# Kernel tuning notes

Hardware: AMD Instinct MI355X
Metric: run time of the kernel (lower is better)

## Reference

```python
import jax, jax.numpy as jnp
import numpy as np

B, L, DH = 4, 4096, 1024
T, DG = 1024, 768
P = 256


def setup_inputs() -> dict:
    key = jax.random.key(0)
    k1, k2, k3, k4, k5 = jax.random.split(key, 5)
    H = jax.random.normal(k1, (B, L, DH), dtype=jnp.float32)
    G = jax.random.normal(k2, (B, T, DG), dtype=jnp.float32)
    # key mask: True = padded/masked. Guarantee at least one valid key per row.
    mask = jax.random.randint(k3, (B, L), 0, 2).astype(jnp.bool_)
    mask = mask.at[:, 0].set(False)
    # torch Linear weights: [out, in]
    Wk_w = jax.random.normal(k4, (P, DH), dtype=jnp.float32) * (DH ** -0.5)
    Wq_w = jax.random.normal(k5, (P, DG), dtype=jnp.float32) * (DG ** -0.5)
    return {"H": H, "G": G, "mask": mask, "Wk_w": Wk_w, "Wq_w": Wq_w}


def reference(H, G, mask, Wk_w, Wq_w):
    # K = Wk(H): [B,L,P]; Q = Wq(G): [B,T,P]
    K = jnp.einsum('bld,pd->blp', H, Wk_w)
    Q = jnp.einsum('btd,pd->btp', G, Wq_w)
    scale = P ** -0.5
    logits = jnp.einsum('btp,blp->btl', Q, K) * scale  # [B,T,L]
    neg_inf = jnp.finfo(logits.dtype).min
    logits = jnp.where(mask[:, None, :], neg_inf, logits)
    alpha = jax.nn.softmax(logits, axis=-1)  # softmax over L (streaming-equivalent)
    Z = jnp.einsum('btl,bld->btd', alpha, H)  # [B,T,DH]
    return Z
```

## Files before the change

### kernel.cpp

```cpp
#include <hip/hip_runtime.h>
#include <hip/hip_bf16.h>


typedef __attribute__((ext_vector_type(8))) short short8;
typedef __attribute__((ext_vector_type(4))) float f32x4;

static __device__ __forceinline__ unsigned short bf16bits(float x) {
    __hip_bfloat16 b = __float2bfloat16(x);
    return *(unsigned short*)&b;
}

static __device__ __forceinline__ void gload_lds16(const __hip_bfloat16* g,
                                                   __hip_bfloat16* l)
{
    auto gp = (const __attribute__((address_space(1))) unsigned int*)(uintptr_t)g;
    auto lp = (__attribute__((address_space(3))) unsigned int*)(unsigned int)(uintptr_t)l;
    __builtin_amdgcn_global_load_lds(gp, lp, 16, 0, 0);
}

__global__ __launch_bounds__(256)
void scan_kernel(const void* __restrict__ mask,
                 unsigned short* __restrict__ idx,
                 int* __restrict__ lc, int* __restrict__ lcpad,
                 float* __restrict__ rowsum, int L, int T, int B)
{
    const int b = blockIdx.x;
    const int tid = threadIdx.x;

    for (int i = tid; i < T; i += 256) rowsum[(long)b * T + i] = 0.f;

    const unsigned char*  m8g  = (const unsigned char*)mask;
    const unsigned short* m16g = (const unsigned short*)mask;
    const unsigned int*   m32g = (const unsigned int*)mask;
    __shared__ int c1, c2, c4, c8, cp, wsh;
    if (tid == 0) { c1 = c2 = c4 = c8 = cp = 0; }
    __syncthreads();
    {
        const int N = B * L;
        int l1 = 0, l2 = 0, l4 = 0, l8 = 0, lp = 0;
        for (int i = tid; i < N; i += 256) l1 += (m8g[i] != 0);
        for (int i = tid; i < N / 2; i += 256) {
            l2 += (m16g[i] != 0);
            lp += ((m8g[2 * i] != 0) == (m8g[2 * i + 1] != 0));
        }
        for (int i = tid; i < N / 4; i += 256) l4 += (m32g[i] != 0);
        for (int i = tid; i < N / 8; i += 256) l8 += ((m32g[2 * i] | m32g[2 * i + 1]) != 0);
        atomicAdd(&c1, l1); atomicAdd(&c2, l2); atomicAdd(&c4, l4);
        atomicAdd(&c8, l8); atomicAdd(&cp, lp);
    }
    __syncthreads();
    if (tid == 0) {
        const float f1 = fabsf(c1 / 16384.f - 0.5f);
        const float f2 = fabsf(c2 / 8192.f  - 0.5f);
        const float f4 = fabsf(c4 / 4096.f  - 0.5f);
        const float f8 = fabsf(c8 / 2048.f  - 0.5f);
        int w = 1; float best = f1;
        if (f2 < best) { best = f2; w = 2; }
        if (f4 < best) { best = f4; w = 4; }
        if (f8 < best) { best = f8; w = 8; }
        if (w == 1 && cp > 7400) w = 2;
        wsh = w;
    }
    __syncthreads();
    const int w = wsh;

    const unsigned char*  m8  = (const unsigned char*)mask;
    const unsigned short* m16 = (const unsigned short*)mask;
    const unsigned int*   m32 = (const unsigned int*)mask;
    const uint2*          m64 = (const uint2*)mask;
    bool v[16];
    int cnt = 0;
    #pragma unroll
    for (int i = 0; i < 16; ++i) {
        const int l = tid * 16 + i;
        const long mi = (long)b * L + l;
        bool masked;
        if (w == 1)      masked = m8[mi] != 0;
        else if (w == 2) masked = m16[mi] != 0;
        else if (w == 4) masked = m32[mi] != 0;
        else             { uint2 q = m64[mi]; masked = (q.x | q.y) != 0; }
        v[i] = !masked;
        cnt += v[i] ? 1 : 0;
    }
    __shared__ int waveTot[4];
    int pre = cnt;
    #pragma unroll
    for (int off = 1; off < 64; off <<= 1) {
        const int t = __shfl_up(pre, off, 64);
        if ((tid & 63) >= off) pre += t;
    }
    if ((tid & 63) == 63) waveTot[tid >> 6] = pre;
    __syncthreads();
    int waveOff = 0;
    for (int wv = 0; wv < (tid >> 6); ++wv) waveOff += waveTot[wv];
    int o = waveOff + pre - cnt;
    #pragma unroll
    for (int i = 0; i < 16; ++i)
        if (v[i]) idx[(long)b * L + (o++)] = (unsigned short)(tid * 16 + i);
    if (tid == 255) {
        const int total = waveOff + pre;
        lc[b] = total;
        lcpad[b] = (total + 127) & ~127;
    }
}

__global__ __launch_bounds__(256)
void prep_all_kernel(const float* __restrict__ H,
                     __hip_bfloat16* __restrict__ Hbf,
                     __hip_bfloat16* __restrict__ Ht,
                     const unsigned short* __restrict__ idx,
                     const int* __restrict__ lc, const int* __restrict__ lcpad,
                     const float* __restrict__ Wk, unsigned short* __restrict__ Wkbf,
                     const float* __restrict__ Wq, unsigned short* __restrict__ Wqbf,
                     const float* __restrict__ G,  unsigned short* __restrict__ Gbf,
                     int L, int D)
{
    __shared__ __align__(16) __hip_bfloat16 tile[64][72];
    int id = blockIdx.x;
    if (id < 4096) {
        const int b  = id >> 10;
        const int c0 = (id & 63) * 64;
        if (c0 >= lcpad[b]) return;
        const int d0 = ((id >> 6) & 15) * 64;
        const int Lcb = lc[b];
        const float* Hb = H + (long)b * L * D;
        __hip_bfloat16* Hbfb = Hbf + (long)b * L * D;
        __hip_bfloat16* Htb  = Ht  + (long)b * D * L;
        const int tx = threadIdx.x & 15, ty = threadIdx.x >> 4;
        #pragma unroll
        for (int p = 0; p < 4; ++p) {
            const int row = ty + p * 16;
            const int c = c0 + row;
            float4 v = {0.f, 0.f, 0.f, 0.f};
            if (c < Lcb) {
                const int l = idx[(long)b * L + c];
                v = *(const float4*)(&Hb[(long)l * D + d0 + tx * 4]);
            }
            ushort4 o;
            o.x = bf16bits(v.x); o.y = bf16bits(v.y);
            o.z = bf16bits(v.z); o.w = bf16bits(v.w);
            *(ushort4*)(&Hbfb[(long)c * D + d0 + tx * 4]) = o;
            tile[tx * 4 + 0][row] = __float2bfloat16(v.x);
            tile[tx * 4 + 1][row] = __float2bfloat16(v.y);
            tile[tx * 4 + 2][row] = __float2bfloat16(v.z);
            tile[tx * 4 + 3][row] = __float2bfloat16(v.w);
        }
        __syncthreads();
        const int ll = threadIdx.x & 7;
        const int dq = threadIdx.x >> 3;
        #pragma unroll
        for (int q = 0; q < 2; ++q) {
            const int dd = dq + q * 32;
            const short8 v = *(const short8*)(&tile[dd][ll * 8]);
            *(short8*)(&Htb[(long)(d0 + dd) * L + c0 + ll * 8]) = v;
        }
        return;
    }
    id -= 4096;
    const float* in; unsigned short* out; int n4;
    if (id < 256)       { in = Wk; out = Wkbf; n4 = (256 * 1024) / 4; }
    else if (id < 448)  { id -= 256; in = Wq; out = Wqbf; n4 = (256 * 768) / 4; }
    else                { id -= 448; in = G;  out = Gbf;  n4 = (4 * 1024 * 768) / 4; }
    const int i = id * 256 + threadIdx.x;
    if (i >= n4) return;
    float4 v = ((const float4*)in)[i];
    ushort4 o;
    o.x = bf16bits(v.x); o.y = bf16bits(v.y);
    o.z = bf16bits(v.z); o.w = bf16bits(v.w);
    ((ushort4*)out)[i] = o;
}

template <typename OutT, int SPLITK, int MODE, int CMODE>
static __device__ __forceinline__
void gemm_bt_body(int bx, int by, int bz, __hip_bfloat16* lds_pool,
                  const __hip_bfloat16* __restrict__ A,
                  const __hip_bfloat16* __restrict__ Bm,
                  OutT* __restrict__ C,
                  int K, int lda, int ldb, int ldc,
                  long batchStrideA, long batchStrideB, long batchStrideC,
                  float scale,
                  float* __restrict__ rowsum, int rowsumStride,
                  long partStride,
                  const int* __restrict__ lc, const int* __restrict__ lcpad,
                  int Lfull)
{
    const int zb = bz / SPLITK;
    const int kc = bz % SPLITK;
    const int rowBase = bx * 128;
    const int colBase = by * 128;

    if constexpr (CMODE == 1) {
        const int bb = rowBase / Lfull;
        if (rowBase - bb * Lfull >= lcpad[bb]) return;
    }
    if constexpr (CMODE == 2) {
        if (colBase >= lcpad[zb]) return;
    }

    A  += (long)zb * batchStrideA;
    Bm += (long)zb * batchStrideB;
    C  += (long)zb * batchStrideC + (long)kc * partStride;
    int Kdyn = K;
    if constexpr (CMODE == 3) Kdyn = lcpad[zb];
    const int Kloc  = Kdyn / SPLITK;
    const int kbase = kc * Kloc;
    const int NT    = Kloc / 32;

    const int tid  = threadIdx.x;
    const int lane = tid & 63;
    const int wave = tid >> 6;
    const int wm = (wave & 1) * 64;
    const int wn = (wave >> 1) * 64;

    __hip_bfloat16* AsP = lds_pool;
    __hip_bfloat16* BsP = lds_pool + 12288;

    f32x4 acc[4][4];
    #pragma unroll
    for (int i = 0; i < 4; ++i)
        #pragma unroll
        for (int j = 0; j < 4; ++j)
            acc[i][j] = (f32x4){0.f, 0.f, 0.f, 0.f};

    const int srow = lane >> 2;
    const int scol = ((lane & 3) ^ ((lane >> 3) & 3)) * 8;
    const long ar0 = (long)(rowBase + wave * 32 + srow) * lda;
    const long ar1 = ar0 + 16l * lda;
    const long br0 = (long)(colBase + wave * 32 + srow) * ldb;
    const long br1 = br0 + 16l * ldb;

    const int mrow = lane & 15;
    const int koff = (((lane >> 4) ^ ((lane >> 1) & 3)) * 8);

    auto stage = [&](int buf, int t) {
        const int kk = kbase + t * 32 + scol;
        gload_lds16(A  + ar0 + kk, AsP + buf * 4096 + wave * 1024);
        gload_lds16(A  + ar1 + kk, AsP + buf * 4096 + wave * 1024 + 512);
        gload_lds16(Bm + br0 + kk, BsP + buf * 4096 + wave * 1024);
        gload_lds16(Bm + br1 + kk, BsP + buf * 4096 + wave * 1024 + 512);
    };

    stage(0, 0);
    if (NT > 1) stage(1, 1);

    int cur = 0;
    for (int t = 0; t < NT; ++t) {
        if (t + 1 < NT)
            asm volatile("s_waitcnt vmcnt(4)" ::: "memory");
        else
            asm volatile("s_waitcnt vmcnt(0)" ::: "memory");
        __builtin_amdgcn_s_barrier();
        if (t + 2 < NT) {
            const int nxt2 = (cur >= 1) ? cur - 1 : cur + 2;
            stage(nxt2, t + 2);
        }

        short8 af[4], bf[4];
        #pragma unroll
        for (int mi = 0; mi < 4; ++mi)
            af[mi] = *(const short8*)(AsP + cur * 4096 + (wm + mi * 16 + mrow) * 32 + koff);
        #pragma unroll
        for (int ni = 0; ni < 4; ++ni)
            bf[ni] = *(const short8*)(BsP + cur * 4096 + (wn + ni * 16 + mrow) * 32 + koff);

        #pragma unroll
        for (int mi = 0; mi < 4; ++mi)
            #pragma unroll
            for (int ni = 0; ni < 4; ++ni)
                acc[mi][ni] = __builtin_amdgcn_mfma_f32_16x16x32_bf16(
                    af[mi], bf[ni], acc[mi][ni], 0, 0, 0);
        cur = (cur == 2) ? 0 : cur + 1;
    }

    const int crow0 = (lane >> 4) * 4;
    const int ccol  = lane & 15;

    if constexpr (MODE == 2 || sizeof(OutT) == 2) {
        __syncthreads();
        __hip_bfloat16* cst = lds_pool;

        if constexpr (MODE == 2) {
            const int lcv = lc[zb];
            bool mk[4];
            #pragma unroll
            for (int ni = 0; ni < 4; ++ni)
                mk[ni] = (colBase + wn + ni * 16 + ccol) >= lcv;
            #pragma unroll
            for (int mi = 0; mi < 4; ++mi) {
                #pragma unroll
                for (int r = 0; r < 4; ++r) {
                    const int row = wm + mi * 16 + crow0 + r;
                    float rs = 0.f;
                    #pragma unroll
                    for (int ni = 0; ni < 4; ++ni) {
                        const int col = wn + ni * 16 + ccol;
                        const float e = mk[ni] ? 0.f
                                               : __expf(acc[mi][ni][r] * scale);
                        const __hip_bfloat16 pb = __float2bfloat16(e);
                        cst[row * 136 + (((col >> 3) ^ (row >> 3)) << 3) + (col & 7)] = pb;
                        rs += __bfloat162float(pb);
                    }
                    rs += __shfl_xor(rs, 1, 64);
                    rs += __shfl_xor(rs, 2, 64);
                    rs += __shfl_xor(rs, 4, 64);
                    rs += __shfl_xor(rs, 8, 64);
                    if ((lane & 15) == 0)
                        atomicAdd(&rowsum[(long)zb * rowsumStride + rowBase + row], rs);
                }
            }
        } else {
            #pragma unroll
            for (int mi = 0; mi < 4; ++mi) {
                #pragma unroll
                for (int ni = 0; ni < 4; ++ni) {
                    #pragma unroll
                    for (int r = 0; r < 4; ++r) {
                        const int row = wm + mi * 16 + crow0 + r;
                        const int col = wn + ni * 16 + ccol;
                        cst[row * 136 + (((col >> 3) ^ (row >> 3)) << 3) + (col & 7)] =
                            __float2bfloat16(acc[mi][ni][r] * scale);
                    }
                }
            }
        }
        __syncthreads();
        const int g   = tid & 15;
        const int r4  = tid >> 4;
        const int lof = ((g ^ r4) << 3);
        #pragma unroll
        for (int k = 0; k < 8; ++k) {
            const int row = r4 * 8 + k;
            const short8 v = *(const short8*)(cst + row * 136 + lof);
            *(short8*)(&((__hip_bfloat16*)C)[(long)(rowBase + row) * ldc + colBase + g * 8]) = v;
        }
    } else {
        #pragma unroll
        for (int mi = 0; mi < 4; ++mi) {
            #pragma unroll
            for (int ni = 0; ni < 4; ++ni) {
                #pragma unroll
                for (int r = 0; r < 4; ++r) {
                    const int row = rowBase + wm + mi * 16 + crow0 + r;
                    const int col = colBase + wn + ni * 16 + ccol;
                    ((float*)C)[(long)row * ldc + col] = acc[mi][ni][r] * scale;
                }
            }
        }
    }
}

static __device__ __forceinline__ void xcd_swizzle(int& bx, int& by, int& bz)
{
    const int nwg = gridDim.x * gridDim.y * gridDim.z;
    bx = blockIdx.x; by = blockIdx.y; bz = blockIdx.z;
    if ((nwg & 7) == 0) {
        int lin = bx + gridDim.x * (by + gridDim.y * bz);
        lin = (lin & 7) * (nwg >> 3) + (lin >> 3);
        bx = lin % gridDim.x;
        const int t = lin / gridDim.x;
        by = t % gridDim.y;
        bz = t / gridDim.y;
    }
}

template <typename OutT, int SPLITK, int MODE, int CMODE>
__global__ __launch_bounds__(256)
void gemm_bt_kernel(const __hip_bfloat16* __restrict__ A,
                    const __hip_bfloat16* __restrict__ Bm,
                    OutT* __restrict__ C,
                    int K, int lda, int ldb, int ldc,
                    long batchStrideA, long batchStrideB, long batchStrideC,
                    float scale,
                    float* __restrict__ rowsum, int rowsumStride,
                    long partStride,
                    const int* __restrict__ lc, const int* __restrict__ lcpad,
                    int Lfull)
{
    __shared__ __align__(16) __hip_bfloat16 lds_pool[24576];
    int bx, by, bz;
    xcd_swizzle(bx, by, bz);
    gemm_bt_body<OutT, SPLITK, MODE, CMODE>(bx, by, bz, lds_pool,
        A, Bm, C, K, lda, ldb, ldc, batchStrideA, batchStrideB, batchStrideC,
        scale, rowsum, rowsumStride, partStride, lc, lcpad, Lfull);
}

__global__ __launch_bounds__(256)
void qk_gemm_kernel(const __hip_bfloat16* __restrict__ Gbf,
                    const __hip_bfloat16* __restrict__ Wqbf,
                    __hip_bfloat16* __restrict__ Qbf,
                    const __hip_bfloat16* __restrict__ Hbf,
                    const __hip_bfloat16* __restrict__ Wkbf,
                    __hip_bfloat16* __restrict__ Kbf,
                    const int* __restrict__ lcpad,
                    int DG_, int DH_, int P_, int L_)
{
    __shared__ __align__(16) __hip_bfloat16 lds_pool[24576];
    int bx, by, bz;
    xcd_swizzle(bx, by, bz);
    if (bx < 32) {
        gemm_bt_body<__hip_bfloat16, 1, 0, 0>(bx, by, 0, lds_pool,
            Gbf, Wqbf, Qbf, DG_, DG_, DG_, P_, 0, 0, 0, 1.0f,
            nullptr, 0, 0, nullptr, nullptr, 0);
    } else {
        gemm_bt_body<__hip_bfloat16, 1, 0, 1>(bx - 32, by, 0, lds_pool,
            Hbf, Wkbf, Kbf, DH_, DH_, DH_, P_, 0, 0, 0, 1.0f,
            nullptr, 0, 0, nullptr, lcpad, L_);
    }
}

__global__ __launch_bounds__(256)
void combine_kernel(const float* __restrict__ Zp,
                    const float* __restrict__ rowsum,
                    float* __restrict__ Z, long partStride)
{
    const int i = blockIdx.x * 256 + threadIdx.x;
    const float4 a = ((const float4*)Zp)[i];
    const float4 b = ((const float4*)(Zp + partStride))[i];
    const float inv = 1.0f / rowsum[i >> 8];
    float4 o;
    o.x = (a.x + b.x) * inv;
    o.y = (a.y + b.y) * inv;
    o.z = (a.z + b.z) * inv;
    o.w = (a.w + b.w) * inv;
    ((float4*)Z)[i] = o;
}

extern "C" void kernel_launch(void* const* d_in, const int* in_sizes, int n_in,
                              void* d_out, int out_size, void* d_ws, size_t ws_size,
                              hipStream_t stream)
{
    constexpr int B = 4, L = 4096, DH = 1024, T = 1024, DG = 768, P = 256;

    const float* H  = (const float*)d_in[0];
    const float* G  = (const float*)d_in[1];
    const void*  mask = d_in[2];
    const float* Wk = (const float*)d_in[3];
    const float* Wq = (const float*)d_in[4];
    for (int i = 0; i < n_in; ++i) {
        switch (in_sizes[i]) {
            case B * L * DH: H    = (const float*)d_in[i]; break;
            case B * T * DG: G    = (const float*)d_in[i]; break;
            case B * L:      mask = d_in[i];               break;
            case P * DH:     Wk   = (const float*)d_in[i]; break;
            case P * DG:     Wq   = (const float*)d_in[i]; break;
        }
    }
    float* Z = (float*)d_out;

    char* ws = (char*)d_ws;
    __hip_bfloat16* Hbf  = (__hip_bfloat16*)ws;
    float*          Zp   = (float*)ws;
    __hip_bfloat16* Ht   = (__hip_bfloat16*)(ws + (32l << 20));
    __hip_bfloat16* Gbf  = (__hip_bfloat16*)(ws + (64l << 20));
    __hip_bfloat16* Qbf  = (__hip_bfloat16*)(ws + (70l << 20));
    __hip_bfloat16* Kbf  = (__hip_bfloat16*)(ws + (72l << 20));
    __hip_bfloat16* Wkbf = (__hip_bfloat16*)(ws + (80l << 20));
    __hip_bfloat16* Wqbf = (__hip_bfloat16*)(ws + (80l << 20) + (512l << 10));
    float*          rowsum    = (float*)(ws + (80l << 20) + (896l << 10));
    int*            lcBuf     = (int*)  (ws + (80l << 20) + (961l << 10));
    int*            lcpadBuf  = (int*)  (ws + (80l << 20) + (961l << 10) + 64);
    unsigned short* idxBuf    = (unsigned short*)(ws + (80l << 20) + (962l << 10));
    __hip_bfloat16* Sb   = (__hip_bfloat16*)(ws + (81l << 20));

    constexpr long ZPART = (long)B * T * DH;

    const dim3 blk(256);

    scan_kernel<<<dim3(B), blk, 0, stream>>>(
        mask, idxBuf, lcBuf, lcpadBuf, rowsum, L, T, B);

    prep_all_kernel<<<dim3(7616), blk, 0, stream>>>(
        H, Hbf, Ht, idxBuf, lcBuf, lcpadBuf,
        Wk, (unsigned short*)Wkbf, Wq, (unsigned short*)Wqbf,
        G, (unsigned short*)Gbf, L, DH);

    qk_gemm_kernel<<<dim3(160, 2, 1), blk, 0, stream>>>(
        Gbf, Wqbf, Qbf, Hbf, Wkbf, Kbf, lcpadBuf, DG, DH, P, L);

    gemm_bt_kernel<__hip_bfloat16, 1, 2, 2><<<dim3(T / 128, L / 128, B), blk, 0, stream>>>(
        Qbf, Kbf, Sb, P, P, P, L,
        (long)T * P, (long)L * P, (long)T * L, 0.0625f,
        rowsum, T, 0, lcBuf, lcpadBuf, L);
    gemm_bt_kernel<float, 2, 0, 3><<<dim3(T / 128, DH / 128, B * 2), blk, 0, stream>>>(
        Sb, Ht, Zp, L, L, L, DH,
        (long)T * L, (long)DH * L, (long)T * DH, 1.0f,
        nullptr, 0, ZPART, nullptr, lcpadBuf, L);
    combine_kernel<<<dim3((B * T * DH / 4) / 256), blk, 0, stream>>>(
        Zp, rowsum, Z, ZPART);
}
```

Before: 219.9 us.

## Fuse mask scan into consumers, drop split-K and combine kernel for Z GEMM

Removes the separate single-block-per-batch scan kernel. Each prep, QK, S and Z block now recomputes the mask width detection and valid-key count (or prefix compaction) itself. The Z GEMM no longer uses split-K plus a combine pass: it uses 64-row tiles with full K and applies the rowsum normalisation in its epilogue, which saves the partial-buffer round trip and two launches. In exchange, every block redundantly reads the whole mask (16K bytes, several passes), which adds latency and memory traffic per block.

```diff
diff --git a/kernel.cpp b/kernel.cpp
--- a/kernel.cpp
+++ b/kernel.cpp
@@ -18,150 +18,154 @@
     __builtin_amdgcn_global_load_lds(gp, lp, 16, 0, 0);
 }
 
-__global__ __launch_bounds__(256)
-void scan_kernel(const void* __restrict__ mask,
-                 unsigned short* __restrict__ idx,
-                 int* __restrict__ lc, int* __restrict__ lcpad,
-                 float* __restrict__ rowsum, int L, int T, int B)
-{
-    const int b = blockIdx.x;
+static __device__ bool masked_at(const void* mask, int w, long i)
+{
+    if (w == 1) return ((const unsigned char*)mask)[i] != 0;
+    if (w == 2) return ((const unsigned short*)mask)[i] != 0;
+    if (w == 4) return ((const unsigned int*)mask)[i] != 0;
+    uint2 q = ((const uint2*)mask)[i]; return (q.x | q.y) != 0;
+}
+
+static __device__ int detect_width_dev(const void* mask, int* sh)
+{
     const int tid = threadIdx.x;
-
-    for (int i = tid; i < T; i += 256) rowsum[(long)b * T + i] = 0.f;
-
-    const unsigned char*  m8g  = (const unsigned char*)mask;
-    const unsigned short* m16g = (const unsigned short*)mask;
-    const unsigned int*   m32g = (const unsigned int*)mask;
-    __shared__ int c1, c2, c4, c8, cp, wsh;
-    if (tid == 0) { c1 = c2 = c4 = c8 = cp = 0; }
-    __syncthreads();
-    {
-        const int N = B * L;
-        int l1 = 0, l2 = 0, l4 = 0, l8 = 0, lp = 0;
-        for (int i = tid; i < N; i += 256) l1 += (m8g[i] != 0);
-        for (int i = tid; i < N / 2; i += 256) {
-            l2 += (m16g[i] != 0);
-            lp += ((m8g[2 * i] != 0) == (m8g[2 * i + 1] != 0));
-        }
-        for (int i = tid; i < N / 4; i += 256) l4 += (m32g[i] != 0);
-        for (int i = tid; i < N / 8; i += 256) l8 += ((m32g[2 * i] | m32g[2 * i + 1]) != 0);
-        atomicAdd(&c1, l1); atomicAdd(&c2, l2); atomicAdd(&c4, l4);
-        atomicAdd(&c8, l8); atomicAdd(&cp, lp);
-    }
-    __syncthreads();
-    if (tid == 0) {
-        const float f1 = fabsf(c1 / 16384.f - 0.5f);
-        const float f2 = fabsf(c2 / 8192.f  - 0.5f);
-        const float f4 = fabsf(c4 / 4096.f  - 0.5f);
-        const float f8 = fabsf(c8 / 2048.f  - 0.5f);
-        int w = 1; float best = f1;
-        if (f2 < best) { best = f2; w = 2; }
-        if (f4 < best) { best = f4; w = 4; }
-        if (f8 < best) { best = f8; w = 8; }
-        if (w == 1 && cp > 7400) w = 2;
-        wsh = w;
-    }
-    __syncthreads();
-    const int w = wsh;
-
     const unsigned char*  m8  = (const unsigned char*)mask;
     const unsigned short* m16 = (const unsigned short*)mask;
     const unsigned int*   m32 = (const unsigned int*)mask;
-    const uint2*          m64 = (const uint2*)mask;
-    bool v[16];
+    if (tid < 5) sh[tid] = 0;
+    __syncthreads();
+    int l1 = 0, l2 = 0, l4 = 0, l8 = 0, lp = 0;
+    for (int i = tid; i < 16384; i += 256) l1 += (m8[i] != 0);
+    for (int i = tid; i < 8192;  i += 256) {
+        l2 += (m16[i] != 0);
+        lp += ((m8[2 * i] != 0) == (m8[2 * i + 1] != 0));
+    }
+    for (int i = tid; i < 4096;  i += 256) l4 += (m32[i] != 0);
+    for (int i = tid; i < 2048;  i += 256) l8 += ((m32[2 * i] | m32[2 * i + 1]) != 0);
+    atomicAdd(&sh[0], l1); atomicAdd(&sh[1], l2); atomicAdd(&sh[2], l4);
+    atomicAdd(&sh[3], l8); atomicAdd(&sh[4], lp);
+    __syncthreads();
+    const float f1 = fabsf(sh[0] / 16384.f - 0.5f);
+    const float f2 = fabsf(sh[1] / 8192.f  - 0.5f);
+    const float f4 = fabsf(sh[2] / 4096.f  - 0.5f);
+    const float f8 = fabsf(sh[3] / 2048.f  - 0.5f);
+    int w = 1; float best = f1;
+    if (f2 < best) { best = f2; w = 2; }
+    if (f4 < best) { best = f4; w = 4; }
+    if (f8 < best) { best = f8; w = 8; }
+    if (w == 1 && sh[4] > 7400) w = 2;
+    return w;
+}
+
+static __device__ int count_valid_dev(const void* mask, int w, int b, int L, int* sh)
+{
+    const int tid = threadIdx.x;
+    if (tid == 0) sh[5] = 0;
+    __syncthreads();
     int cnt = 0;
+    for (int i = tid; i < L; i += 256)
+        cnt += masked_at(mask, w, (long)b * L + i) ? 0 : 1;
     #pragma unroll
-    for (int i = 0; i < 16; ++i) {
-        const int l = tid * 16 + i;
-        const long mi = (long)b * L + l;
-        bool masked;
-        if (w == 1)      masked = m8[mi] != 0;
-        else if (w == 2) masked = m16[mi] != 0;
-        else if (w == 4) masked = m32[mi] != 0;
-        else             { uint2 q = m64[mi]; masked = (q.x | q.y) != 0; }
-        v[i] = !masked;
-        cnt += v[i] ? 1 : 0;
-    }
-    __shared__ int waveTot[4];
-    int pre = cnt;
-    #pragma unroll
-    for (int off = 1; off < 64; off <<= 1) {
-        const int t = __shfl_up(pre, off, 64);
-        if ((tid & 63) >= off) pre += t;
-    }
-    if ((tid & 63) == 63) waveTot[tid >> 6] = pre;
+    for (int off = 32; off; off >>= 1) cnt += __shfl_xor(cnt, off, 64);
+    if ((tid & 63) == 0) atomicAdd(&sh[5], cnt);
     __syncthreads();
-    int waveOff = 0;
-    for (int wv = 0; wv < (tid >> 6); ++wv) waveOff += waveTot[wv];
-    int o = waveOff + pre - cnt;
-    #pragma unroll
-    for (int i = 0; i < 16; ++i)
-        if (v[i]) idx[(long)b * L + (o++)] = (unsigned short)(tid * 16 + i);
-    if (tid == 255) {
-        const int total = waveOff + pre;
-        lc[b] = total;
-        lcpad[b] = (total + 127) & ~127;
-    }
+    return sh[5];
 }
 
 __global__ __launch_bounds__(256)
 void prep_all_kernel(const float* __restrict__ H,
                      __hip_bfloat16* __restrict__ Hbf,
                      __hip_bfloat16* __restrict__ Ht,
-                     const unsigned short* __restrict__ idx,
-                     const int* __restrict__ lc, const int* __restrict__ lcpad,
+                     const void* __restrict__ mask,
                      const float* __restrict__ Wk, unsigned short* __restrict__ Wkbf,
                      const float* __restrict__ Wq, unsigned short* __restrict__ Wqbf,
                      const float* __restrict__ G,  unsigned short* __restrict__ Gbf,
+                     float* __restrict__ rowsum,
                      int L, int D)
 {
     __shared__ __align__(16) __hip_bfloat16 tile[64][72];
+    __shared__ unsigned short sidx[4096];
+    __shared__ int sh[8];
     int id = blockIdx.x;
+    const int tid = threadIdx.x;
     if (id < 4096) {
         const int b  = id >> 10;
         const int c0 = (id & 63) * 64;
-        if (c0 >= lcpad[b]) return;
         const int d0 = ((id >> 6) & 15) * 64;
-        const int Lcb = lc[b];
+
+        const int w = detect_width_dev(mask, sh);
+        bool v[16];
+        int cnt = 0;
+        #pragma unroll
+        for (int i = 0; i < 16; ++i) {
+            const int l = tid * 16 + i;
+            v[i] = !masked_at(mask, w, (long)b * L + l);
+            cnt += v[i] ? 1 : 0;
+        }
+        int pre = cnt;
+        #pragma unroll
+        for (int off = 1; off < 64; off <<= 1) {
+            const int t = __shfl_up(pre, off, 64);
+            if ((tid & 63) >= off) pre += t;
+        }
+        __syncthreads();
+        if ((tid & 63) == 63) sh[tid >> 6] = pre;
+        __syncthreads();
+        int waveOff = 0;
+        for (int wv = 0; wv < (tid >> 6); ++wv) waveOff += sh[wv];
+        int o = waveOff + pre - cnt;
+        #pragma unroll
+        for (int i = 0; i < 16; ++i)
+            if (v[i]) sidx[o++] = (unsigned short)(tid * 16 + i);
+        if (tid == 255) sh[6] = waveOff + pre;
+        __syncthreads();
+        const int Lcb = sh[6];
+        const int lcpadb = (Lcb + 127) & ~127;
+        if (c0 >= lcpadb) return;
+
         const float* Hb = H + (long)b * L * D;
         __hip_bfloat16* Hbfb = Hbf + (long)b * L * D;
         __hip_bfloat16* Htb  = Ht  + (long)b * D * L;
-        const int tx = threadIdx.x & 15, ty = threadIdx.x >> 4;
+        const int tx = tid & 15, ty = tid >> 4;
         #pragma unroll
         for (int p = 0; p < 4; ++p) {
             const int row = ty + p * 16;
             const int c = c0 + row;
-            float4 v = {0.f, 0.f, 0.f, 0.f};
+            float4 vv = {0.f, 0.f, 0.f, 0.f};
             if (c < Lcb) {
-                const int l = idx[(long)b * L + c];
-                v = *(const float4*)(&Hb[(long)l * D + d0 + tx * 4]);
+                const int l = sidx[c];
+                vv = *(const float4*)(&Hb[(long)l * D + d0 + tx * 4]);
             }
-            ushort4 o;
-            o.x = bf16bits(v.x); o.y = bf16bits(v.y);
-            o.z = bf16bits(v.z); o.w = bf16bits(v.w);
-            *(ushort4*)(&Hbfb[(long)c * D + d0 + tx * 4]) = o;
-            tile[tx * 4 + 0][row] = __float2bfloat16(v.x);
-            tile[tx * 4 + 1][row] = __float2bfloat16(v.y);
-            tile[tx * 4 + 2][row] = __float2bfloat16(v.z);
-            tile[tx * 4 + 3][row] = __float2bfloat16(v.w);
-        }
-        __syncthreads();
-        const int ll = threadIdx.x & 7;
-        const int dq = threadIdx.x >> 3;
+            ushort4 oo;
+            oo.x = bf16bits(vv.x); oo.y = bf16bits(vv.y);
+            oo.z = bf16bits(vv.z); oo.w = bf16bits(vv.w);
+            *(ushort4*)(&Hbfb[(long)c * D + d0 + tx * 4]) = oo;
+            tile[tx * 4 + 0][row] = __float2bfloat16(vv.x);
+            tile[tx * 4 + 1][row] = __float2bfloat16(vv.y);
+            tile[tx * 4 + 2][row] = __float2bfloat16(vv.z);
+            tile[tx * 4 + 3][row] = __float2bfloat16(vv.w);
+        }
+        __syncthreads();
+        const int ll = tid & 7;
+        const int dq = tid >> 3;
         #pragma unroll
         for (int q = 0; q < 2; ++q) {
             const int dd = dq + q * 32;
-            const short8 v = *(const short8*)(&tile[dd][ll * 8]);
-            *(short8*)(&Htb[(long)(d0 + dd) * L + c0 + ll * 8]) = v;
+            const short8 vv = *(const short8*)(&tile[dd][ll * 8]);
+            *(short8*)(&Htb[(long)(d0 + dd) * L + c0 + ll * 8]) = vv;
         }
         return;
     }
     id -= 4096;
+    if (id >= 3520) {
+        rowsum[(id - 3520) * 256 + tid] = 0.f;
+        return;
+    }
     const float* in; unsigned short* out; int n4;
     if (id < 256)       { in = Wk; out = Wkbf; n4 = (256 * 1024) / 4; }
     else if (id < 448)  { id -= 256; in = Wq; out = Wqbf; n4 = (256 * 768) / 4; }
     else                { id -= 448; in = G;  out = Gbf;  n4 = (4 * 1024 * 768) / 4; }
-    const int i = id * 256 + threadIdx.x;
+    const int i = id * 256 + tid;
     if (i >= n4) return;
     float4 v = ((const float4*)in)[i];
     ushort4 o;
@@ -170,61 +174,47 @@
     ((ushort4*)out)[i] = o;
 }
 
-template <typename OutT, int SPLITK, int MODE, int CMODE>
+template <typename OutT, int MODE, int BM>
 static __device__ __forceinline__
-void gemm_bt_body(int bx, int by, int bz, __hip_bfloat16* lds_pool,
+void gemm_bt_body(int bx, int by, int zb, __hip_bfloat16* lds_pool,
                   const __hip_bfloat16* __restrict__ A,
                   const __hip_bfloat16* __restrict__ Bm,
                   OutT* __restrict__ C,
                   int K, int lda, int ldb, int ldc,
                   long batchStrideA, long batchStrideB, long batchStrideC,
                   float scale,
-                  float* __restrict__ rowsum, int rowsumStride,
-                  long partStride,
-                  const int* __restrict__ lc, const int* __restrict__ lcpad,
-                  int Lfull)
-{
-    const int zb = bz / SPLITK;
-    const int kc = bz % SPLITK;
-    const int rowBase = bx * 128;
-    const int colBase = by * 128;
-
-    if constexpr (CMODE == 1) {
-        const int bb = rowBase / Lfull;
-        if (rowBase - bb * Lfull >= lcpad[bb]) return;
-    }
-    if constexpr (CMODE == 2) {
-        if (colBase >= lcpad[zb]) return;
-    }
+                  float* __restrict__ rowsum, int rowsumStride, int lcv)
+{
+    constexpr int MI  = BM / 32;
+    constexpr int ACH = BM / 64;
+    constexpr int ATS = BM * 32;
 
     A  += (long)zb * batchStrideA;
     Bm += (long)zb * batchStrideB;
-    C  += (long)zb * batchStrideC + (long)kc * partStride;
-    int Kdyn = K;
-    if constexpr (CMODE == 3) Kdyn = lcpad[zb];
-    const int Kloc  = Kdyn / SPLITK;
-    const int kbase = kc * Kloc;
-    const int NT    = Kloc / 32;
+    C  += (long)zb * batchStrideC;
+    const int NT = K / 32;
 
     const int tid  = threadIdx.x;
     const int lane = tid & 63;
     const int wave = tid >> 6;
-    const int wm = (wave & 1) * 64;
+    const int wm = (wave & 1) * (BM / 2);
     const int wn = (wave >> 1) * 64;
+    const int rowBase = bx * BM;
+    const int colBase = by * 128;
 
     __hip_bfloat16* AsP = lds_pool;
-    __hip_bfloat16* BsP = lds_pool + 12288;
-
-    f32x4 acc[4][4];
+    __hip_bfloat16* BsP = lds_pool + 3 * ATS;
+
+    f32x4 acc[MI][4];
     #pragma unroll
-    for (int i = 0; i < 4; ++i)
+    for (int i = 0; i < MI; ++i)
         #pragma unroll
         for (int j = 0; j < 4; ++j)
             acc[i][j] = (f32x4){0.f, 0.f, 0.f, 0.f};
 
     const int srow = lane >> 2;
     const int scol = ((lane & 3) ^ ((lane >> 3) & 3)) * 8;
-    const long ar0 = (long)(rowBase + wave * 32 + srow) * lda;
+    const long ar0 = (long)(rowBase + wave * (BM / 4) + srow) * lda;
     const long ar1 = ar0 + 16l * lda;
     const long br0 = (long)(colBase + wave * 32 + srow) * ldb;
     const long br1 = br0 + 16l * ldb;
@@ -233,38 +223,43 @@
     const int koff = (((lane >> 4) ^ ((lane >> 1) & 3)) * 8);
 
     auto stage = [&](int buf, int t) {
-        const int kk = kbase + t * 32 + scol;
-        gload_lds16(A  + ar0 + kk, AsP + buf * 4096 + wave * 1024);
-        gload_lds16(A  + ar1 + kk, AsP + buf * 4096 + wave * 1024 + 512);
+        const int kk = t * 32 + scol;
+        gload_lds16(A + ar0 + kk, AsP + buf * ATS + wave * (BM / 4) * 32);
+        if constexpr (ACH == 2)
+            gload_lds16(A + ar1 + kk, AsP + buf * ATS + wave * (BM / 4) * 32 + 512);
         gload_lds16(Bm + br0 + kk, BsP + buf * 4096 + wave * 1024);
         gload_lds16(Bm + br1 + kk, BsP + buf * 4096 + wave * 1024 + 512);
     };
 
     stage(0, 0);
-    if (NT > 1) stage(1, 1);
+    stage(1, 1);
 
     int cur = 0;
     for (int t = 0; t < NT; ++t) {
-        if (t + 1 < NT)
-            asm volatile("s_waitcnt vmcnt(4)" ::: "memory");
-        else
+        if (t + 1 < NT) {
+            if constexpr (ACH == 2)
+                asm volatile("s_waitcnt vmcnt(4)" ::: "memory");
+            else
+                asm volatile("s_waitcnt vmcnt(3)" ::: "memory");
+        } else {
             asm volatile("s_waitcnt vmcnt(0)" ::: "memory");
+        }
         __builtin_amdgcn_s_barrier();
         if (t + 2 < NT) {
             const int nxt2 = (cur >= 1) ? cur - 1 : cur + 2;
             stage(nxt2, t + 2);
         }
 
-        short8 af[4], bf[4];
-        #pragma unroll
-        for (int mi = 0; mi < 4; ++mi)
-            af[mi] = *(const short8*)(AsP + cur * 4096 + (wm + mi * 16 + mrow) * 32 + koff);
+        short8 af[MI], bf[4];
+        #pragma unroll
+        for (int mi = 0; mi < MI; ++mi)
+            af[mi] = *(const short8*)(AsP + cur * ATS + (wm + mi * 16 + mrow) * 32 + koff);
         #pragma unroll
         for (int ni = 0; ni < 4; ++ni)
             bf[ni] = *(const short8*)(BsP + cur * 4096 + (wn + ni * 16 + mrow) * 32 + koff);
 
         #pragma unroll
-        for (int mi = 0; mi < 4; ++mi)
+        for (int mi = 0; mi < MI; ++mi)
             #pragma unroll
             for (int ni = 0; ni < 4; ++ni)
                 acc[mi][ni] = __builtin_amdgcn_mfma_f32_16x16x32_bf16(
@@ -275,52 +270,34 @@
     const int crow0 = (lane >> 4) * 4;
     const int ccol  = lane & 15;
 
-    if constexpr (MODE == 2 || sizeof(OutT) == 2) {
+    if constexpr (MODE == 2) {
         __syncthreads();
         __hip_bfloat16* cst = lds_pool;
-
-        if constexpr (MODE == 2) {
-            const int lcv = lc[zb];
-            bool mk[4];
+        bool mk[4];
+        #pragma unroll
+        for (int ni = 0; ni < 4; ++ni)
+            mk[ni] = (colBase + wn + ni * 16 + ccol) >= lcv;
+        #pragma unroll
+        for (int mi = 0; mi < MI; ++mi) {
             #pragma unroll
-            for (int ni = 0; ni < 4; ++ni)
-                mk[ni] = (colBase + wn + ni * 16 + ccol) >= lcv;
-            #pragma unroll
-            for (int mi = 0; mi < 4; ++mi) {
-                #pragma unroll
-                for (int r = 0; r < 4; ++r) {
-                    const int row = wm + mi * 16 + crow0 + r;
-                    float rs = 0.f;
-                    #pragma unroll
-                    for (int ni = 0; ni < 4; ++ni) {
-                        const int col = wn + ni * 16 + ccol;
-                        const float e = mk[ni] ? 0.f
-                                               : __expf(acc[mi][ni][r] * scale);
-                        const __hip_bfloat16 pb = __float2bfloat16(e);
-                        cst[row * 136 + (((col >> 3) ^ (row >> 3)) << 3) + (col & 7)] = pb;
-                        rs += __bfloat162float(pb);
-                    }
-                    rs += __shfl_xor(rs, 1, 64);
-                    rs += __shfl_xor(rs, 2, 64);
-                    rs += __shfl_xor(rs, 4, 64);
-                    rs += __shfl_xor(rs, 8, 64);
-                    if ((lane & 15) == 0)
-                        atomicAdd(&rowsum[(long)zb * rowsumStride + rowBase + row], rs);
-                }
-            }
-        } else {
-            #pragma unroll
-            for (int mi = 0; mi < 4; ++mi) {
+            for (int r = 0; r < 4; ++r) {
+                const int row = wm + mi * 16 + crow0 + r;
+                float rs = 0.f;
                 #pragma unroll
                 for (int ni = 0; ni < 4; ++ni) {
-                    #pragma unroll
-                    for (int r = 0; r < 4; ++r) {
-                        const int row = wm + mi * 16 + crow0 + r;
-                        const int col = wn + ni * 16 + ccol;
-                        cst[row * 136 + (((col >> 3) ^ (row >> 3)) << 3) + (col & 7)] =
-                            __float2bfloat16(acc[mi][ni][r] * scale);
-                    }
+                    const int col = wn + ni * 16 + ccol;
+                    const float e = mk[ni] ? 0.f
+                                           : __expf(acc[mi][ni][r] * scale);
+                    const __hip_bfloat16 pb = __float2bfloat16(e);
+                    cst[row * 136 + (((col >> 3) ^ (row >> 3)) << 3) + (col & 7)] = pb;
+                    rs += __bfloat162float(pb);
                 }
+                rs += __shfl_xor(rs, 1, 64);
+                rs += __shfl_xor(rs, 2, 64);
+                rs += __shfl_xor(rs, 4, 64);
+                rs += __shfl_xor(rs, 8, 64);
+                if ((lane & 15) == 0)
+                    atomicAdd(&rowsum[(long)zb * rowsumStride + rowBase + row], rs);
             }
         }
         __syncthreads();
@@ -333,9 +310,49 @@
             const short8 v = *(const short8*)(cst + row * 136 + lof);
             *(short8*)(&((__hip_bfloat16*)C)[(long)(rowBase + row) * ldc + colBase + g * 8]) = v;
         }
+    } else if constexpr (MODE == 3) {
+        #pragma unroll
+        for (int mi = 0; mi < MI; ++mi) {
+            #pragma unroll
+            for (int r = 0; r < 4; ++r) {
+                const int row = rowBase + wm + mi * 16 + crow0 + r;
+                const float inv = 1.0f / rowsum[(long)zb * rowsumStride + row];
+                #pragma unroll
+                for (int ni = 0; ni < 4; ++ni) {
+                    const int col = colBase + wn + ni * 16 + ccol;
+                    ((float*)C)[(long)row * ldc + col] = acc[mi][ni][r] * inv;
+                }
+            }
+        }
+    } else if constexpr (sizeof(OutT) == 2) {
+        __syncthreads();
+        __hip_bfloat16* cst = lds_pool;
+        #pragma unroll
+        for (int mi = 0; mi < MI; ++mi) {
+            #pragma unroll
+            for (int ni = 0; ni < 4; ++ni) {
+                #pragma unroll
+                for (int r = 0; r < 4; ++r) {
+                    const int row = wm + mi * 16 + crow0 + r;
+                    const int col = wn + ni * 16 + ccol;
+                    cst[row * 136 + (((col >> 3) ^ (row >> 3)) << 3) + (col & 7)] =
+                        __float2bfloat16(acc[mi][ni][r] * scale);
+                }
+            }
+        }
+        __syncthreads();
+        const int g   = tid & 15;
+        const int r4  = tid >> 4;
+        const int lof = ((g ^ r4) << 3);
+        #pragma unroll
+        for (int k = 0; k < 8; ++k) {
+            const int row = r4 * 8 + k;
+            const short8 v = *(const short8*)(cst + row * 136 + lof);
+            *(short8*)(&((__hip_bfloat16*)C)[(long)(rowBase + row) * ldc + colBase + g * 8]) = v;
+        }
     } else {
         #pragma unroll
-        for (int mi = 0; mi < 4; ++mi) {
+        for (int mi = 0; mi < MI; ++mi) {
             #pragma unroll
             for (int ni = 0; ni < 4; ++ni) {
                 #pragma unroll
@@ -363,27 +380,6 @@
     }
 }
 
-template <typename OutT, int SPLITK, int MODE, int CMODE>
-__global__ __launch_bounds__(256)
-void gemm_bt_kernel(const __hip_bfloat16* __restrict__ A,
-                    const __hip_bfloat16* __restrict__ Bm,
-                    OutT* __restrict__ C,
-                    int K, int lda, int ldb, int ldc,
-                    long batchStrideA, long batchStrideB, long batchStrideC,
-                    float scale,
-                    float* __restrict__ rowsum, int rowsumStride,
-                    long partStride,
-                    const int* __restrict__ lc, const int* __restrict__ lcpad,
-                    int Lfull)
-{
-    __shared__ __align__(16) __hip_bfloat16 lds_pool[24576];
-    int bx, by, bz;
-    xcd_swizzle(bx, by, bz);
-    gemm_bt_body<OutT, SPLITK, MODE, CMODE>(bx, by, bz, lds_pool,
-        A, Bm, C, K, lda, ldb, ldc, batchStrideA, batchStrideB, batchStrideC,
-        scale, rowsum, rowsumStride, partStride, lc, lcpad, Lfull);
-}
-
 __global__ __launch_bounds__(256)
 void qk_gemm_kernel(const __hip_bfloat16* __restrict__ Gbf,
                     const __hip_bfloat16* __restrict__ Wqbf,
@@ -391,38 +387,74 @@
                     const __hip_bfloat16* __restrict__ Hbf,
                     const __hip_bfloat16* __restrict__ Wkbf,
                     __hip_bfloat16* __restrict__ Kbf,
-                    const int* __restrict__ lcpad,
+                    const void* __restrict__ mask,
                     int DG_, int DH_, int P_, int L_)
 {
     __shared__ __align__(16) __hip_bfloat16 lds_pool[24576];
     int bx, by, bz;
     xcd_swizzle(bx, by, bz);
     if (bx < 32) {
-        gemm_bt_body<__hip_bfloat16, 1, 0, 0>(bx, by, 0, lds_pool,
+        gemm_bt_body<__hip_bfloat16, 0, 128>(bx, by, 0, lds_pool,
             Gbf, Wqbf, Qbf, DG_, DG_, DG_, P_, 0, 0, 0, 1.0f,
-            nullptr, 0, 0, nullptr, nullptr, 0);
+            nullptr, 0, 0);
     } else {
-        gemm_bt_body<__hip_bfloat16, 1, 0, 1>(bx - 32, by, 0, lds_pool,
+        int* sh = (int*)lds_pool;
+        const int w = detect_width_dev(mask, sh);
+        const int rowBase = (bx - 32) * 128;
+        const int bb = rowBase / L_;
+        const int cnt = count_valid_dev(mask, w, bb, L_, sh);
+        const int lcpadb = (cnt + 127) & ~127;
+        __syncthreads();
+        if (rowBase - bb * L_ >= lcpadb) return;
+        gemm_bt_body<__hip_bfloat16, 0, 128>(bx - 32, by, 0, lds_pool,
             Hbf, Wkbf, Kbf, DH_, DH_, DH_, P_, 0, 0, 0, 1.0f,
-            nullptr, 0, 0, nullptr, lcpad, L_);
+            nullptr, 0, 0);
     }
 }
 
 __global__ __launch_bounds__(256)
-void combine_kernel(const float* __restrict__ Zp,
-                    const float* __restrict__ rowsum,
-                    float* __restrict__ Z, long partStride)
-{
-    const int i = blockIdx.x * 256 + threadIdx.x;
-    const float4 a = ((const float4*)Zp)[i];
-    const float4 b = ((const float4*)(Zp + partStride))[i];
-    const float inv = 1.0f / rowsum[i >> 8];
-    float4 o;
-    o.x = (a.x + b.x) * inv;
-    o.y = (a.y + b.y) * inv;
-    o.z = (a.z + b.z) * inv;
-    o.w = (a.w + b.w) * inv;
-    ((float4*)Z)[i] = o;
+void s_gemm_kernel(const __hip_bfloat16* __restrict__ Qbf,
+                   const __hip_bfloat16* __restrict__ Kbf,
+                   __hip_bfloat16* __restrict__ Sb,
+                   const void* __restrict__ mask,
+                   float* __restrict__ rowsum,
+                   int P_, int L_, int T_)
+{
+    __shared__ __align__(16) __hip_bfloat16 lds_pool[24576];
+    int bx, by, bz;
+    xcd_swizzle(bx, by, bz);
+    int* sh = (int*)lds_pool;
+    const int w = detect_width_dev(mask, sh);
+    const int lcv = count_valid_dev(mask, w, bz, L_, sh);
+    const int lcpadb = (lcv + 127) & ~127;
+    __syncthreads();
+    if (by * 128 >= lcpadb) return;
+    gemm_bt_body<__hip_bfloat16, 2, 128>(bx, by, bz, lds_pool,
+        Qbf, Kbf, Sb, P_, P_, P_, L_,
+        (long)T_ * P_, (long)L_ * P_, (long)T_ * L_, 0.0625f,
+        rowsum, T_, lcv);
+}
+
+__global__ __launch_bounds__(256)
+void z_gemm_kernel(const __hip_bfloat16* __restrict__ Sb,
+                   const __hip_bfloat16* __restrict__ Ht,
+                   float* __restrict__ Z,
+                   const void* __restrict__ mask,
+                   const float* __restrict__ rowsum,
+                   int L_, int DH_, int T_)
+{
+    __shared__ __align__(16) __hip_bfloat16 lds_pool[24576];
+    int bx, by, bz;
+    xcd_swizzle(bx, by, bz);
+    int* sh = (int*)lds_pool;
+    const int w = detect_width_dev(mask, sh);
+    const int cnt = count_valid_dev(mask, w, bz, L_, sh);
+    const int Kdyn = (cnt + 127) & ~127;
+    __syncthreads();
+    gemm_bt_body<float, 3, 64>(bx, by, bz, lds_pool,
+        Sb, Ht, Z, Kdyn, L_, L_, DH_,
+        (long)T_ * L_, (long)DH_ * L_, (long)T_ * DH_, 1.0f,
+        (float*)rowsum, T_, 0);
 }
 
 extern "C" void kernel_launch(void* const* d_in, const int* in_sizes, int n_in,
@@ -449,42 +481,28 @@
 
     char* ws = (char*)d_ws;
     __hip_bfloat16* Hbf  = (__hip_bfloat16*)ws;
-    float*          Zp   = (float*)ws;
     __hip_bfloat16* Ht   = (__hip_bfloat16*)(ws + (32l << 20));
     __hip_bfloat16* Gbf  = (__hip_bfloat16*)(ws + (64l << 20));
     __hip_bfloat16* Qbf  = (__hip_bfloat16*)(ws + (70l << 20));
     __hip_bfloat16* Kbf  = (__hip_bfloat16*)(ws + (72l << 20));
     __hip_bfloat16* Wkbf = (__hip_bfloat16*)(ws + (80l << 20));
     __hip_bfloat16* Wqbf = (__hip_bfloat16*)(ws + (80l << 20) + (512l << 10));
-    float*          rowsum    = (float*)(ws + (80l << 20) + (896l << 10));
-    int*            lcBuf     = (int*)  (ws + (80l << 20) + (961l << 10));
-    int*            lcpadBuf  = (int*)  (ws + (80l << 20) + (961l << 10) + 64);
-    unsigned short* idxBuf    = (unsigned short*)(ws + (80l << 20) + (962l << 10));
+    float*          rowsum = (float*)(ws + (80l << 20) + (896l << 10));
     __hip_bfloat16* Sb   = (__hip_bfloat16*)(ws + (81l << 20));
 
-    constexpr long ZPART = (long)B * T * DH;
-
     const dim3 blk(256);
 
-    scan_kernel<<<dim3(B), blk, 0, stream>>>(
-        mask, idxBuf, lcBuf, lcpadBuf, rowsum, L, T, B);
-
-    prep_all_kernel<<<dim3(7616), blk, 0, stream>>>(
-        H, Hbf, Ht, idxBuf, lcBuf, lcpadBuf,
+    prep_all_kernel<<<dim3(7632), blk, 0, stream>>>(
+        H, Hbf, Ht, mask,
         Wk, (unsigned short*)Wkbf, Wq, (unsigned short*)Wqbf,
-        G, (unsigned short*)Gbf, L, DH);
+        G, (unsigned short*)Gbf, rowsum, L, DH);
 
     qk_gemm_kernel<<<dim3(160, 2, 1), blk, 0, stream>>>(
-        Gbf, Wqbf, Qbf, Hbf, Wkbf, Kbf, lcpadBuf, DG, DH, P, L);
-
-    gemm_bt_kernel<__hip_bfloat16, 1, 2, 2><<<dim3(T / 128, L / 128, B), blk, 0, stream>>>(
-        Qbf, Kbf, Sb, P, P, P, L,
-        (long)T * P, (long)L * P, (long)T * L, 0.0625f,
-        rowsum, T, 0, lcBuf, lcpadBuf, L);
-    gemm_bt_kernel<float, 2, 0, 3><<<dim3(T / 128, DH / 128, B * 2), blk, 0, stream>>>(
-        Sb, Ht, Zp, L, L, L, DH,
-        (long)T * L, (long)DH * L, (long)T * DH, 1.0f,
-        nullptr, 0, ZPART, nullptr, lcpadBuf, L);
-    combine_kernel<<<dim3((B * T * DH / 4) / 256), blk, 0, stream>>>(
-        Zp, rowsum, Z, ZPART);
-}
+        Gbf, Wqbf, Qbf, Hbf, Wkbf, Kbf, mask, DG, DH, P, L);
+
+    s_gemm_kernel<<<dim3(T / 128, L / 128, B), blk, 0, stream>>>(
+        Qbf, Kbf, Sb, mask, rowsum, P, L, T);
+
+    z_gemm_kernel<<<dim3(T / 64, DH / 128, B), blk, 0, stream>>>(
+        Sb, Ht, Z, mask, rowsum, L, DH, T);
+}
```

Measured after the change: 363.0 us. 65.1% more time.
